# Kernel tuning notes

Hardware: AMD Instinct MI355X
Metric: run time of the kernel (lower is better)

Reference implementation:

```python
import jax, jax.numpy as jnp
import numpy as np

N_QUBITS = 8
N_LAYERS = 1
DIM = 1 << N_QUBITS  # 256 statevector amplitudes; PennyLane wire 0 = most significant bit

_idx = np.arange(DIM)
_BITS = np.stack([(_idx >> (N_QUBITS - 1 - w)) & 1 for w in range(N_QUBITS)])  # (n, D)
_FLIP = np.stack([_idx ^ (1 << (N_QUBITS - 1 - w)) for w in range(N_QUBITS)])  # (n, D)

def _cnot_perm(c, t):
    return _idx ^ (((_idx >> (N_QUBITS - 1 - c)) & 1) << (N_QUBITS - 1 - t))

_CNOT_NP = [_cnot_perm(w, w + 1) for w in range(N_QUBITS - 1)] + [_cnot_perm(N_QUBITS - 1, 0)]
BITS = jnp.asarray(_BITS)
FLIP = jnp.asarray(_FLIP)
CNOTS = [jnp.asarray(p) for p in _CNOT_NP]


def _ry(t):
    c = jnp.cos(t / 2)
    s = jnp.sin(t / 2)
    return jnp.stack([jnp.stack([c, -s], -1), jnp.stack([s, c], -1)], -2).astype(jnp.complex64)


def _rx(t):
    c = jnp.cos(t / 2).astype(jnp.complex64)
    s = (-1j) * jnp.sin(t / 2).astype(jnp.complex64)
    return jnp.stack([jnp.stack([c, s], -1), jnp.stack([s, c], -1)], -2)


def _rz(t):
    tc = t.astype(jnp.complex64)
    e0 = jnp.exp(-0.5j * tc)
    e1 = jnp.exp(0.5j * tc)
    z = jnp.zeros_like(e0)
    return jnp.stack([jnp.stack([e0, z], -1), jnp.stack([z, e1], -1)], -2)


def _apply(state, U, w):
    # state: (B, 2**n) complex64; U: (2,2) shared or (B,2,2) per-sample; wire w (MSB-first)
    B = state.shape[0]
    s = state.reshape(B, 1 << w, 2, -1)
    if U.ndim == 3:
        s = jnp.einsum('bij,bajc->baic', U, s)
    else:
        s = jnp.einsum('ij,bajc->baic', U, s)
    return s.reshape(B, DIM)


def _circuit(angles, weights):
    # angles: (B, n_qubits) float32; weights: (n_layers, n_qubits, 3) float32
    B = angles.shape[0]
    state = jnp.zeros((B, DIM), jnp.complex64).at[:, 0].set(1.0)
    for w in range(N_QUBITS):
        state = _apply(state, _ry(angles[:, w]), w)  # per-sample RY encoding
    for l in range(N_LAYERS):
        for w in range(N_QUBITS):
            state = _apply(state, _rx(weights[l, w, 0]), w)
            state = _apply(state, _ry(weights[l, w, 1]), w)
            state = _apply(state, _rz(weights[l, w, 2]), w)
        for p in CNOTS:  # CNOT ring entangler as basis permutation
            state = state[:, p]
    probs = jnp.abs(state) ** 2
    outs = []
    for w in range(N_QUBITS):
        overlap = jnp.conj(state) * state[:, FLIP[w]]
        sign = (1.0 - 2.0 * BITS[w]).astype(probs.dtype)
        outs.append(jnp.sum(jnp.real(overlap), -1))       # <X_w>
        outs.append(jnp.sum(sign * jnp.imag(overlap), -1))  # <Y_w>
        outs.append(jnp.sum(sign * probs, -1))            # <Z_w>
    return jnp.stack(outs, -1)  # (B, 3*n_qubits), order X0,Y0,Z0,X1,...


def setup_inputs() -> dict:
    key = jax.random.key(0)
    k1, k2, k3 = jax.random.split(key, 3)
    B, IN_DIM = 16384, 512
    h = jax.random.normal(k1, (B, IN_DIM), jnp.float32)
    W_pre = 0.02 * jax.random.normal(k2, (N_QUBITS, IN_DIM), jnp.float32)
    b_pre = jnp.zeros((N_QUBITS,), jnp.float32)
    weights = 0.01 * jax.random.normal(k3, (N_LAYERS, N_QUBITS, 3), jnp.float32)
    return {"h": h, "W_pre": W_pre, "b_pre": b_pre, "weights": weights}


def reference(h, W_pre, b_pre, weights):
    a = h @ W_pre.T + b_pre
    a = jnp.clip(jnp.tanh(a) * (jnp.pi / 2), -jnp.pi, jnp.pi)  # _scale_to_angles
    z = _circuit(a, weights)
    norm = jnp.linalg.norm(z, axis=-1, keepdims=True)
    return z / jnp.maximum(norm, 1e-12)  # F.normalize(dim=-1)
```

## Files before the change

kernel.cpp:

```cpp
#include <hip/hip_runtime.h>


__global__ __launch_bounds__(256) void vqc_gemv(
    const float* __restrict__ h,
    const float* __restrict__ Wp,
    float* __restrict__ aw,
    int B)
{
    const int lane = threadIdx.x & 63;
    const int wave = (blockIdx.x * blockDim.x + threadIdx.x) >> 6;
    const int nwv  = (gridDim.x * blockDim.x) >> 6;

    const float4* W4 = (const float4*)Wp;
    float wf[8][8];
    #pragma unroll
    for (int q = 0; q < 8; ++q) {
        float4 v0 = W4[q * 128 + lane * 2 + 0];
        float4 v1 = W4[q * 128 + lane * 2 + 1];
        wf[q][0] = v0.x; wf[q][1] = v0.y; wf[q][2] = v0.z; wf[q][3] = v0.w;
        wf[q][4] = v1.x; wf[q][5] = v1.y; wf[q][6] = v1.z; wf[q][7] = v1.w;
    }

    const int b3 = (lane >> 3) & 1, b4 = (lane >> 4) & 1, b5 = (lane >> 5) & 1;
    const float4* H4 = (const float4*)h;

    const int row0 = wave * 2;
    if (row0 >= B) return;

    float4 h00 = H4[row0 * 128 + lane * 2 + 0];
    float4 h01 = H4[row0 * 128 + lane * 2 + 1];
    int row1 = row0 + 1;
    float4 h10 = H4[(row1 < B ? row1 : row0) * 128 + lane * 2 + 0];
    float4 h11 = H4[(row1 < B ? row1 : row0) * 128 + lane * 2 + 1];

    float hf0[8] = { h00.x, h00.y, h00.z, h00.w, h01.x, h01.y, h01.z, h01.w };
    float hf1[8] = { h10.x, h10.y, h10.z, h10.w, h11.x, h11.y, h11.z, h11.w };

    float acc0[8], acc1[8];
    #pragma unroll
    for (int q = 0; q < 8; ++q) {
        float a0 = 0.f, a1 = 0.f;
        #pragma unroll
        for (int j = 0; j < 8; ++j) {
            a0 = fmaf(wf[q][j], hf0[j], a0);
            a1 = fmaf(wf[q][j], hf1[j], a1);
        }
        acc0[q] = a0; acc1[q] = a1;
    }

    float n0[4], n1[4];
    #pragma unroll
    for (int j = 0; j < 4; ++j) {
        float k0 = b3 ? acc0[1 + 2*j] : acc0[0 + 2*j];
        float s0 = b3 ? acc0[0 + 2*j] : acc0[1 + 2*j];
        float k1 = b3 ? acc1[1 + 2*j] : acc1[0 + 2*j];
        float s1 = b3 ? acc1[0 + 2*j] : acc1[1 + 2*j];
        n0[j] = k0 + __shfl_xor(s0, 8);
        n1[j] = k1 + __shfl_xor(s1, 8);
    }
    float m0[2], m1[2];
    #pragma unroll
    for (int i = 0; i < 2; ++i) {
        float k0 = b4 ? n0[1 + 2*i] : n0[0 + 2*i];
        float s0 = b4 ? n0[0 + 2*i] : n0[1 + 2*i];
        float k1 = b4 ? n1[1 + 2*i] : n1[0 + 2*i];
        float s1 = b4 ? n1[0 + 2*i] : n1[1 + 2*i];
        m0[i] = k0 + __shfl_xor(s0, 16);
        m1[i] = k1 + __shfl_xor(s1, 16);
    }
    float v0, v1;
    {
        float k0 = b5 ? m0[1] : m0[0];
        float s0 = b5 ? m0[0] : m0[1];
        float k1 = b5 ? m1[1] : m1[0];
        float s1 = b5 ? m1[0] : m1[1];
        v0 = k0 + __shfl_xor(s0, 32);
        v1 = k1 + __shfl_xor(s1, 32);
    }
    v0 += __shfl_xor(v0, 1); v1 += __shfl_xor(v1, 1);
    v0 += __shfl_xor(v0, 2); v1 += __shfl_xor(v1, 2);
    v0 += __shfl_xor(v0, 4); v1 += __shfl_xor(v1, 4);

    if ((lane & 7) == 0) {
        int q = lane >> 3;
        aw[row0 * 8 + q] = v0;
        if (row1 < B) aw[row1 * 8 + q] = v1;
    }
}

__global__ __launch_bounds__(256) void vqc_epilogue(
    const float* __restrict__ aw,
    const float* __restrict__ bp,
    const float* __restrict__ wt,
    float* __restrict__ out,
    int B)
{
    const int row = blockIdx.x * blockDim.x + threadIdx.x;
    if (row >= B) return;

    const float4* A4 = (const float4*)aw;
    float4 a0 = A4[row * 2 + 0];
    float4 a1 = A4[row * 2 + 1];
    float av[8] = { a0.x, a0.y, a0.z, a0.w, a1.x, a1.y, a1.z, a1.w };

    float X[8], Y[8], Z[8];
    #pragma unroll
    for (int q = 0; q < 8; ++q) {
        float t0 = wt[q * 3 + 0] * 0.5f;
        float t1 = wt[q * 3 + 1] * 0.5f;
        float t2 = wt[q * 3 + 2] * 0.5f;
        float s0, c0, s1, c1, sz, cz;
        __sincosf(t0, &s0, &c0);
        __sincosf(t1, &s1, &c1);
        __sincosf(t2, &sz, &cz);
        float N00r =  c1 * c0, N00i =  s1 * s0;
        float N01r = -s1 * c0, N01i = -c1 * s0;
        float N10r =  s1 * c0, N10i = -c1 * s0;
        float N11r =  c1 * c0, N11i = -s1 * s0;
        float M00r = cz * N00r + sz * N00i, M00i = cz * N00i - sz * N00r;
        float M01r = cz * N01r + sz * N01i, M01i = cz * N01i - sz * N01r;
        float M10r = cz * N10r - sz * N10i, M10i = cz * N10i + sz * N10r;
        float M11r = cz * N11r - sz * N11i, M11i = cz * N11i + sz * N11r;

        float a = av[q] + bp[q];
        a = fminf(fmaxf(a, -15.f), 15.f);
        float e = __expf(a + a);
        float th = (e - 1.f) / (e + 1.f);
        float phi = th * 0.78539816339744831f;
        float ss, cc;
        __sincosf(phi, &ss, &cc);
        float ar = M00r * cc + M01r * ss, ai = M00i * cc + M01i * ss;
        float br = M10r * cc + M11r * ss, bi = M10i * cc + M11i * ss;
        Z[q] = (ar * ar + ai * ai) - (br * br + bi * bi);
        X[q] = 2.f * (ar * br + ai * bi);
        Y[q] = 2.f * (ar * bi - ai * br);
    }

    float P[8], T[8];
    P[0] = Z[0];
    #pragma unroll
    for (int w = 1; w < 8; ++w) P[w] = P[w - 1] * Z[w];
    T[7] = Z[7];
    #pragma unroll
    for (int w = 6; w >= 0; --w) T[w] = Z[w] * T[w + 1];
    float Z2to6 = Z[2] * Z[3] * Z[4] * Z[5] * Z[6];

    float o[24];
    #pragma unroll
    for (int w = 0; w < 7; ++w) o[3 * w] = X[w] * X[w + 1];
    o[21] = X[7] * X[0] * X[1];
    o[1] = X[0] * Y[1] * T[2];
    #pragma unroll
    for (int w = 1; w < 7; ++w) o[3 * w + 1] = Y[w] * X[w + 1] * P[w - 1];
    o[22] = -Y[7] * Y[0] * Y[1] * Z2to6;
    o[2] = T[1];
    #pragma unroll
    for (int w = 1; w < 8; ++w) o[3 * w + 2] = P[w];

    float sq = 0.f;
    #pragma unroll
    for (int j = 0; j < 24; ++j) sq = fmaf(o[j], o[j], sq);
    float inv = 1.f / fmaxf(sqrtf(sq), 1e-12f);

    float4* O4 = (float4*)(out + row * 24);
    #pragma unroll
    for (int j = 0; j < 6; ++j) {
        float4 vv = { o[4 * j] * inv, o[4 * j + 1] * inv,
                      o[4 * j + 2] * inv, o[4 * j + 3] * inv };
        O4[j] = vv;
    }
}

extern "C" void kernel_launch(void* const* d_in, const int* in_sizes, int n_in,
                              void* d_out, int out_size, void* d_ws, size_t ws_size,
                              hipStream_t stream) {
    const float* h  = (const float*)d_in[0];
    const float* Wp = (const float*)d_in[1];
    const float* bp = (const float*)d_in[2];
    const float* wt = (const float*)d_in[3];
    float* out = (float*)d_out;
    float* aw  = (float*)d_ws;

    const int B = in_sizes[0] / 512;
    const int nblk1 = (B + 511) / 512;
    vqc_gemv<<<nblk1 * 128, 256, 0, stream>>>(h, Wp, aw, B);
    vqc_epilogue<<<(B + 255) / 256, 256, 0, stream>>>(aw, bp, wt, out, B);
}
```

Baseline: 83.23 us.

## Fuse GEMV and circuit epilogue into a single kernel via wave shuffles

Merges the projection GEMV and the analytic circuit epilogue into one kernel. The per-row pre-activations are passed between lanes with shuffles instead of being written to and read back from a workspace buffer. This removes a second kernel launch and the intermediate global round trip. In exchange, every lane in the wave redundantly computes the trig-heavy epilogue while only two lanes store results, so the epilogue compute grows about 32-fold.

```diff
diff --git a/kernel.cpp b/kernel.cpp
--- a/kernel.cpp
+++ b/kernel.cpp
@@ -1,35 +1,36 @@
 #include <hip/hip_runtime.h>
 
 
-__global__ __launch_bounds__(256) void vqc_gemv(
+__global__ __launch_bounds__(256) void vqc_fused(
     const float* __restrict__ h,
     const float* __restrict__ Wp,
-    float* __restrict__ aw,
+    const float* __restrict__ bp,
+    const float* __restrict__ wt,
+    float* __restrict__ out,
     int B)
 {
     const int lane = threadIdx.x & 63;
     const int wave = (blockIdx.x * blockDim.x + threadIdx.x) >> 6;
-    const int nwv  = (gridDim.x * blockDim.x) >> 6;
+
+    const int row0 = wave * 2;
+    if (row0 >= B) return;
+    const int row1 = row0 + 1;
 
     const float4* W4 = (const float4*)Wp;
     float wf[8][8];
     #pragma unroll
     for (int q = 0; q < 8; ++q) {
-        float4 v0 = W4[q * 128 + lane * 2 + 0];
-        float4 v1 = W4[q * 128 + lane * 2 + 1];
-        wf[q][0] = v0.x; wf[q][1] = v0.y; wf[q][2] = v0.z; wf[q][3] = v0.w;
-        wf[q][4] = v1.x; wf[q][5] = v1.y; wf[q][6] = v1.z; wf[q][7] = v1.w;
+        float4 w0 = W4[q * 128 + lane * 2 + 0];
+        float4 w1 = W4[q * 128 + lane * 2 + 1];
+        wf[q][0] = w0.x; wf[q][1] = w0.y; wf[q][2] = w0.z; wf[q][3] = w0.w;
+        wf[q][4] = w1.x; wf[q][5] = w1.y; wf[q][6] = w1.z; wf[q][7] = w1.w;
     }
 
     const int b3 = (lane >> 3) & 1, b4 = (lane >> 4) & 1, b5 = (lane >> 5) & 1;
     const float4* H4 = (const float4*)h;
 
-    const int row0 = wave * 2;
-    if (row0 >= B) return;
-
     float4 h00 = H4[row0 * 128 + lane * 2 + 0];
     float4 h01 = H4[row0 * 128 + lane * 2 + 1];
-    int row1 = row0 + 1;
     float4 h10 = H4[(row1 < B ? row1 : row0) * 128 + lane * 2 + 0];
     float4 h11 = H4[(row1 < B ? row1 : row0) * 128 + lane * 2 + 1];
 
@@ -81,27 +82,11 @@
     v0 += __shfl_xor(v0, 2); v1 += __shfl_xor(v1, 2);
     v0 += __shfl_xor(v0, 4); v1 += __shfl_xor(v1, 4);
 
-    if ((lane & 7) == 0) {
-        int q = lane >> 3;
-        aw[row0 * 8 + q] = v0;
-        if (row1 < B) aw[row1 * 8 + q] = v1;
-    }
-}
-
-__global__ __launch_bounds__(256) void vqc_epilogue(
-    const float* __restrict__ aw,
-    const float* __restrict__ bp,
-    const float* __restrict__ wt,
-    float* __restrict__ out,
-    int B)
-{
-    const int row = blockIdx.x * blockDim.x + threadIdx.x;
-    if (row >= B) return;
-
-    const float4* A4 = (const float4*)aw;
-    float4 a0 = A4[row * 2 + 0];
-    float4 a1 = A4[row * 2 + 1];
-    float av[8] = { a0.x, a0.y, a0.z, a0.w, a1.x, a1.y, a1.z, a1.w };
+    const int r = lane & 1;
+    float vsel = r ? v1 : v0;
+    float av[8];
+    #pragma unroll
+    for (int q = 0; q < 8; ++q) av[q] = __shfl(vsel, q * 8 + r);
 
     float X[8], Y[8], Z[8];
     #pragma unroll
@@ -162,12 +147,17 @@
     for (int j = 0; j < 24; ++j) sq = fmaf(o[j], o[j], sq);
     float inv = 1.f / fmaxf(sqrtf(sq), 1e-12f);
 
-    float4* O4 = (float4*)(out + row * 24);
-    #pragma unroll
-    for (int j = 0; j < 6; ++j) {
-        float4 vv = { o[4 * j] * inv, o[4 * j + 1] * inv,
-                      o[4 * j + 2] * inv, o[4 * j + 3] * inv };
-        O4[j] = vv;
+    if (lane < 2) {
+        const int row = row0 + lane;
+        if (row < B) {
+            float4* O4 = (float4*)(out + row * 24);
+            #pragma unroll
+            for (int j = 0; j < 6; ++j) {
+                float4 vv = { o[4 * j] * inv, o[4 * j + 1] * inv,
+                              o[4 * j + 2] * inv, o[4 * j + 3] * inv };
+                O4[j] = vv;
+            }
+        }
     }
 }
 
@@ -179,10 +169,9 @@
     const float* bp = (const float*)d_in[2];
     const float* wt = (const float*)d_in[3];
     float* out = (float*)d_out;
-    float* aw  = (float*)d_ws;
+    (void)d_ws; (void)ws_size;
 
     const int B = in_sizes[0] / 512;
-    const int nblk1 = (B + 511) / 512;
-    vqc_gemv<<<nblk1 * 128, 256, 0, stream>>>(h, Wp, aw, B);
-    vqc_epilogue<<<(B + 255) / 256, 256, 0, stream>>>(aw, bp, wt, out, B);
+    const int nblk = (B + 7) / 8;
+    vqc_fused<<<nblk, 256, 0, stream>>>(h, Wp, bp, wt, out, B);
 }
```

Result: slower. 95.14 us (+14.3%).
